# Kernel optimization log

Measured on AMD Instinct MI355X. Metric: run time of the kernel, lower is better.

The kernel has to match this reference:

```python
import jax, jax.numpy as jnp
import numpy as np

NEG_SLOPE = 0.2  # PyG GATConv default negative_slope


def gat_conv(x, src, dst, W, att_src, att_dst, bias, heads):
    """PyG-style GATConv (concat=True). src/dst already include self-loops.
    x: [N, Fin]; W: [Fin, heads*Fout]; att_*: [heads, Fout]; bias: [heads*Fout].
    """
    N = x.shape[0]
    Fout = att_src.shape[-1]
    h = (x @ W).reshape(N, heads, Fout)              # [N, H, C]
    a_s = jnp.einsum('nhc,hc->nh', h, att_src)        # [N, H]
    a_d = jnp.einsum('nhc,hc->nh', h, att_dst)        # [N, H]
    e = jax.nn.leaky_relu(a_s[src] + a_d[dst], NEG_SLOPE)   # [E, H]
    # segment softmax over destination nodes
    m = jax.lax.stop_gradient(jax.ops.segment_max(e, dst, num_segments=N))  # [N, H]
    ex = jnp.exp(e - m[dst])
    denom = jax.ops.segment_sum(ex, dst, num_segments=N)     # [N, H]
    alpha = ex / (denom[dst] + 1e-16)                          # [E, H]
    msg = h[src] * alpha[:, :, None]                           # [E, H, C]
    out = jax.ops.segment_sum(msg, dst, num_segments=N)       # [N, H, C]
    return out.reshape(N, heads * Fout) + bias


def setup_inputs() -> dict:
    key = jax.random.key(0)
    ks = jax.random.split(key, 16)
    NU, NS, D, H, CTX, B, E = 100000, 100000, 64, 2, 3, 512, 1600000
    inp = {
        'user_idx': jax.random.randint(ks[0], (B,), 0, NU),
        'context_idx': jax.random.randint(ks[1], (B, CTX), 0, NS),
        'edge_index': jax.random.randint(ks[2], (2, E), 0, NS),
        'user_emb': jax.random.normal(ks[3], (NU, D), jnp.float32),
        'service_emb': jax.random.normal(ks[4], (NS, D), jnp.float32),
        'W1': jax.random.normal(ks[5], (D, H * D), jnp.float32) / np.sqrt(D),
        'att_src1': jax.random.normal(ks[6], (H, D), jnp.float32) / np.sqrt(D),
        'att_dst1': jax.random.normal(ks[7], (H, D), jnp.float32) / np.sqrt(D),
        'b1': jnp.zeros((H * D,), jnp.float32),
        'W2': jax.random.normal(ks[8], (H * D, D), jnp.float32) / np.sqrt(H * D),
        'att_src2': jax.random.normal(ks[9], (1, D), jnp.float32) / np.sqrt(D),
        'att_dst2': jax.random.normal(ks[10], (1, D), jnp.float32) / np.sqrt(D),
        'b2': jnp.zeros((D,), jnp.float32),
        'fc_w': jax.random.normal(ks[11], (D * (CTX + 1), NS), jnp.float32) / np.sqrt(D * (CTX + 1)),
        'fc_b': jnp.zeros((NS,), jnp.float32),
    }
    return inp


def reference(user_idx, context_idx, edge_index, user_emb, service_emb,
              W1, att_src1, att_dst1, b1, W2, att_src2, att_dst2, b2, fc_w, fc_b):
    N = service_emb.shape[0]
    loops = jnp.arange(N)
    src = jnp.concatenate([edge_index[0], loops])  # add self loops (PyG default)
    dst = jnp.concatenate([edge_index[1], loops])
    user_vec = user_emb[user_idx]                                  # [B, D]
    g = gat_conv(service_emb, src, dst, W1, att_src1, att_dst1, b1, heads=2)
    g = jax.nn.elu(g)
    g = gat_conv(g, src, dst, W2, att_src2, att_dst2, b2, heads=1)  # [N, D]
    ctx = g[context_idx]                                            # [B, CTX, D]
    ctx = ctx.reshape(ctx.shape[0], -1)
    x = jnp.concatenate([user_vec, ctx], axis=1)                    # [B, D*(CTX+1)]
    return x @ fc_w + fc_b                                           # [B, num_services]
```

## Files before the change

kernel.cpp:

```cpp
#include <hip/hip_runtime.h>
#include <hip/hip_bf16.h>
#include <math.h>

#define NEG_SLOPE 0.2f

#define NPB 512
#define NPB_SH 9
#define SRC_BITS 18
#define LCAP 16384
#define BCAP 16384

typedef __attribute__((ext_vector_type(8))) short short8;
typedef __attribute__((ext_vector_type(4))) float f32x4;

__device__ __forceinline__ float leaky(float x) { return x > 0.f ? x : NEG_SLOPE * x; }

__device__ __forceinline__ unsigned short f2bf(float f) {
  unsigned u = __float_as_uint(f);
  unsigned r = (u + 0x7FFFu + ((u >> 16) & 1u)) >> 16;
  return (unsigned short)r;
}

__global__ void k_h1(const float* __restrict__ x, const float* __restrict__ W1,
                     const float* __restrict__ att_src, const float* __restrict__ att_dst,
                     unsigned short* __restrict__ h1, float* __restrict__ a_s,
                     float* __restrict__ a_d, int N) {
  __shared__ __align__(16) float W1s[64 * 128];
  __shared__ __align__(16) float xs[2][64];
  for (int i = threadIdx.x; i < 64 * 128; i += 256) W1s[i] = W1[i];
  const int ln  = threadIdx.x >> 7;
  const int col = threadIdx.x & 127;
  const int head = col >> 6;
  const int c = col & 63;
  const float as_w = att_src[head * 64 + c];
  const float ad_w = att_dst[head * 64 + c];
  __syncthreads();
  float wreg[64];
#pragma unroll
  for (int cc = 0; cc < 64; ++cc) wreg[cc] = W1s[cc * 128 + col];

  const int node0 = blockIdx.x * 32;
  for (int it = 0; it < 16; ++it) {
    const int nbase = node0 + it * 2;
    __syncthreads();
    if (threadIdx.x < 128) {
      const int nn = nbase + (threadIdx.x >> 6);
      if (nn < N) xs[threadIdx.x >> 6][threadIdx.x & 63] = x[(size_t)nn * 64 + (threadIdx.x & 63)];
    }
    __syncthreads();
    const int n = nbase + ln;
    if (n >= N) continue;
    float acc = 0.f;
#pragma unroll
    for (int q = 0; q < 16; ++q) {
      const float4 xv = *(const float4*)&xs[ln][q * 4];
      acc = fmaf(xv.x, wreg[q * 4 + 0], acc);
      acc = fmaf(xv.y, wreg[q * 4 + 1], acc);
      acc = fmaf(xv.z, wreg[q * 4 + 2], acc);
      acc = fmaf(xv.w, wreg[q * 4 + 3], acc);
    }
    h1[(size_t)n * 128 + col] = f2bf(acc);
    float vs = acc * as_w;
    float vd = acc * ad_w;
#pragma unroll
    for (int off = 32; off > 0; off >>= 1) {
      vs += __shfl_down(vs, off, 64);
      vd += __shfl_down(vd, off, 64);
    }
    if (c == 0) { a_s[n * 2 + head] = vs; a_d[n * 2 + head] = vd; }
  }
}

__global__ void k_binit(int* __restrict__ cursor, int NB) {
  const int i = blockIdx.x * 256 + threadIdx.x;
  if (i < NB) cursor[i] = i * BCAP;
}

__global__ __launch_bounds__(1024) void k_bscatter(const int* __restrict__ src,
                                                   const int* __restrict__ dst, int E, int Etot,
                                                   int epb, int* __restrict__ cursor,
                                                   unsigned* __restrict__ rec, int NB) {
  __shared__ int hist[256];
  __shared__ int cur[256];
  const int tid = threadIdx.x;
  if (tid < 256) hist[tid] = 0;
  __syncthreads();
  const int e0 = blockIdx.x * epb;
  const int e1 = min(e0 + epb, Etot);
  for (int e = e0 + tid; e < e1; e += 1024) {
    const int d = (e < E) ? dst[e] : (e - E);
    atomicAdd(&hist[d >> NPB_SH], 1);
  }
  __syncthreads();
  if (tid < NB) {
    const int c = hist[tid];
    cur[tid] = c ? atomicAdd(&cursor[tid], c) : 0;
  }
  __syncthreads();
  for (int e = e0 + tid; e < e1; e += 1024) {
    int sv, d;
    if (e < E) { sv = src[e]; d = dst[e]; } else { sv = d = e - E; }
    const int b = d >> NPB_SH;
    const int p = atomicAdd(&cur[b], 1);
    rec[p] = (unsigned)sv | ((unsigned)(d & (NPB - 1)) << SRC_BITS);
  }
}

__global__ void k_bscan2(const int* __restrict__ cursor, int* __restrict__ bucketBase,
                         int NB, int Etot, int* __restrict__ rowptr, int N) {
  __shared__ int s[256];
  const int tid = threadIdx.x;
  const int v = (tid < NB) ? (cursor[tid] - tid * BCAP) : 0;
  s[tid] = v;
  __syncthreads();
  for (int off = 1; off < 256; off <<= 1) {
    const int t = (tid >= off) ? s[tid - off] : 0;
    __syncthreads();
    s[tid] += t;
    __syncthreads();
  }
  if (tid < NB) bucketBase[tid] = s[tid] - v;
  if (tid == 0) { bucketBase[NB] = Etot; rowptr[N] = Etot; }
}

__global__ __launch_bounds__(1024) void k_bcsr(const unsigned* __restrict__ rec,
                                               const int* __restrict__ bucketBase,
                                               int* __restrict__ rowptr, int* __restrict__ adj,
                                               int N, int NB) {
  __shared__ int ldeg[NPB];
  __shared__ int s[NPB];
  __shared__ int ladj[LCAP];
  const int b = blockIdx.x;
  const int tid = threadIdx.x;
  const int o0 = bucketBase[b];
  const int cnt = bucketBase[b + 1] - o0;
  const int r0 = b * BCAP;
  if (tid < NPB) ldeg[tid] = 0;
  __syncthreads();
  for (int i = tid; i < cnt; i += 1024)
    atomicAdd(&ldeg[rec[r0 + i] >> SRC_BITS], 1);
  __syncthreads();
  int v = 0;
  if (tid < NPB) { v = ldeg[tid]; s[tid] = v; }
  __syncthreads();
  for (int off = 1; off < NPB; off <<= 1) {
    int t = 0;
    if (tid < NPB && tid >= off) t = s[tid - off];
    __syncthreads();
    if (tid < NPB) s[tid] += t;
    __syncthreads();
  }
  if (tid < NPB) {
    const int excl = s[tid] - v;
    const int node = b * NPB + tid;
    if (node < N) rowptr[node] = o0 + excl;
    ldeg[tid] = excl;
  }
  __syncthreads();
  if (cnt <= LCAP) {
    for (int i = tid; i < cnt; i += 1024) {
      const unsigned r = rec[r0 + i];
      const int p = atomicAdd(&ldeg[r >> SRC_BITS], 1);
      ladj[p] = (int)(r & ((1u << SRC_BITS) - 1));
    }
    __syncthreads();
    for (int i = tid; i < cnt; i += 1024) adj[o0 + i] = ladj[i];
  } else {
    for (int i = tid; i < cnt; i += 1024) {
      const unsigned r = rec[r0 + i];
      const int p = atomicAdd(&ldeg[r >> SRC_BITS], 1);
      adj[o0 + p] = (int)(r & ((1u << SRC_BITS) - 1));
    }
  }
}

__global__ void k_zeroflags(int* __restrict__ flagC, int* __restrict__ flag1,
                            int* __restrict__ cnt, int N) {
  const int i = blockIdx.x * 256 + threadIdx.x;
  if (i < N) { flagC[i] = 0; flag1[i] = 0; }
  if (i < 2) cnt[i] = 0;
}

__global__ void k_markC(const int* __restrict__ ctx, int nctx, int* __restrict__ flagC,
                        int* __restrict__ flag1, int* __restrict__ listC,
                        int* __restrict__ list1, int* __restrict__ cnt) {
  const int i = blockIdx.x * 256 + threadIdx.x;
  if (i >= nctx) return;
  const int n = ctx[i];
  if (atomicExch(&flagC[n], 1) == 0) {
    listC[atomicAdd(&cnt[0], 1)] = n;
    if (atomicExch(&flag1[n], 1) == 0)
      list1[atomicAdd(&cnt[1], 1)] = n;
  }
}

__global__ void k_markS1(const int* __restrict__ listC, const int* __restrict__ rowptr,
                         const int* __restrict__ adj, int* __restrict__ flag1,
                         int* __restrict__ list1, int* __restrict__ cnt) {
  const int i = blockIdx.x * 256 + threadIdx.x;
  if (i >= cnt[0]) return;
  const int n = listC[i];
  const int kb = rowptr[n], ke = rowptr[n + 1];
  for (int k = kb; k < ke; ++k) {
    const int s = adj[k];
    if (atomicExch(&flag1[s], 1) == 0)
      list1[atomicAdd(&cnt[1], 1)] = s;
  }
}

__global__ void k_gat1(const unsigned short* __restrict__ h1, const float* __restrict__ as1,
                       const float* __restrict__ ad1, const int* __restrict__ rowptr,
                       const int* __restrict__ adj, const float* __restrict__ b1,
                       float* __restrict__ g, const int* __restrict__ list1,
                       const int* __restrict__ cnt) {
  const int w = threadIdx.x >> 6;
  const int l = threadIdx.x & 63;
  const int idx = blockIdx.x * 4 + w;
  if (idx >= cnt[1]) return;
  const int n = list1[idx];
  const int half = l >> 5;
  const int q = l & 31;
  const int head = q >> 4;
  const float adh = ad1[n * 2 + head];
  float a0 = 0.f, a1 = 0.f, a2 = 0.f, a3 = 0.f, dsum = 0.f;
  const int kb = rowptr[n], ke = rowptr[n + 1];
  const int kend = ke - 1;
  for (int k = kb + half; k < ke; k += 8) {
    const int e1 = k + 2, e2 = k + 4, e3 = k + 6;
    const int s0 = adj[k];
    const int s1 = adj[min(e1, kend)];
    const int s2 = adj[min(e2, kend)];
    const int s3 = adj[min(e3, kend)];
    const float x0 = as1[s0 * 2 + head] + adh;
    const float x1 = as1[s1 * 2 + head] + adh;
    const float x2 = as1[s2 * 2 + head] + adh;
    const float x3 = as1[s3 * 2 + head] + adh;
    const uint2 u0 = *(const uint2*)(h1 + (size_t)s0 * 128 + 4 * q);
    const uint2 u1 = *(const uint2*)(h1 + (size_t)s1 * 128 + 4 * q);
    const uint2 u2 = *(const uint2*)(h1 + (size_t)s2 * 128 + 4 * q);
    const uint2 u3 = *(const uint2*)(h1 + (size_t)s3 * 128 + 4 * q);
    const float w0 = __expf(leaky(x0));
    const float w1 = (e1 < ke) ? __expf(leaky(x1)) : 0.f;
    const float w2 = (e2 < ke) ? __expf(leaky(x2)) : 0.f;
    const float w3 = (e3 < ke) ? __expf(leaky(x3)) : 0.f;
    dsum += (w0 + w1) + (w2 + w3);
    a0 = fmaf(w0, __uint_as_float(u0.x << 16), a0);
    a1 = fmaf(w0, __uint_as_float(u0.x & 0xFFFF0000u), a1);
    a2 = fmaf(w0, __uint_as_float(u0.y << 16), a2);
    a3 = fmaf(w0, __uint_as_float(u0.y & 0xFFFF0000u), a3);
    a0 = fmaf(w1, __uint_as_float(u1.x << 16), a0);
    a1 = fmaf(w1, __uint_as_float(u1.x & 0xFFFF0000u), a1);
    a2 = fmaf(w1, __uint_as_float(u1.y << 16), a2);
    a3 = fmaf(w1, __uint_as_float(u1.y & 0xFFFF0000u), a3);
    a0 = fmaf(w2, __uint_as_float(u2.x << 16), a0);
    a1 = fmaf(w2, __uint_as_float(u2.x & 0xFFFF0000u), a1);
    a2 = fmaf(w2, __uint_as_float(u2.y << 16), a2);
    a3 = fmaf(w2, __uint_as_float(u2.y & 0xFFFF0000u), a3);
    a0 = fmaf(w3, __uint_as_float(u3.x << 16), a0);
    a1 = fmaf(w3, __uint_as_float(u3.x & 0xFFFF0000u), a1);
    a2 = fmaf(w3, __uint_as_float(u3.y << 16), a2);
    a3 = fmaf(w3, __uint_as_float(u3.y & 0xFFFF0000u), a3);
  }
  a0 += __shfl_xor(a0, 32, 64);
  a1 += __shfl_xor(a1, 32, 64);
  a2 += __shfl_xor(a2, 32, 64);
  a3 += __shfl_xor(a3, 32, 64);
  dsum += __shfl_xor(dsum, 32, 64);
  if (half == 0) {
    const float inv = 1.f / (dsum + 1e-16f);
    const float4 bv = *(const float4*)(b1 + 4 * q);
    float g0 = fmaf(a0, inv, bv.x);
    float g1 = fmaf(a1, inv, bv.y);
    float g2v = fmaf(a2, inv, bv.z);
    float g3 = fmaf(a3, inv, bv.w);
    g0 = g0 > 0.f ? g0 : expm1f(g0);
    g1 = g1 > 0.f ? g1 : expm1f(g1);
    g2v = g2v > 0.f ? g2v : expm1f(g2v);
    g3 = g3 > 0.f ? g3 : expm1f(g3);
    *(float4*)(g + (size_t)n * 128 + 4 * q) = make_float4(g0, g1, g2v, g3);
  }
}

__global__ void k_h2(const float* __restrict__ g, const float* __restrict__ W2,
                     const float* __restrict__ att_s, const float* __restrict__ att_d,
                     unsigned short* __restrict__ h2, float* __restrict__ a_s,
                     float* __restrict__ a_d, const int* __restrict__ list1,
                     const int* __restrict__ cnt) {
  const int cnt1 = cnt[1];
  const int base0 = blockIdx.x * 32;
  if (base0 >= cnt1) return;
  __shared__ __align__(16) float W2s[128 * 64];
  __shared__ __align__(16) float gs[2][128];
  __shared__ float part[2][64];
  for (int i = threadIdx.x; i < 128 * 64; i += 256) W2s[i] = W2[i];
  const int col = threadIdx.x & 63;
  const int kh  = (threadIdx.x >> 6) & 1;
  const int ln  = threadIdx.x >> 7;
  const float as_w = att_s[col], ad_w = att_d[col];
  __syncthreads();
  float wreg[64];
#pragma unroll
  for (int cc = 0; cc < 64; ++cc) wreg[cc] = W2s[(kh * 64 + cc) * 64 + col];

  for (int it = 0; it < 16; ++it) {
    const int sbase = base0 + it * 2;
    __syncthreads();
    {
      const int slot = sbase + (threadIdx.x >> 7);
      if (slot < cnt1) {
        const int nn = list1[slot];
        gs[threadIdx.x >> 7][threadIdx.x & 127] = g[(size_t)nn * 128 + (threadIdx.x & 127)];
      }
    }
    __syncthreads();
    const int slot = sbase + ln;
    const int n = (slot < cnt1) ? list1[slot] : -1;
    float acc = 0.f;
    if (n >= 0) {
#pragma unroll
      for (int q = 0; q < 16; ++q) {
        const float4 gv = *(const float4*)&gs[ln][kh * 64 + q * 4];
        acc = fmaf(gv.x, wreg[q * 4 + 0], acc);
        acc = fmaf(gv.y, wreg[q * 4 + 1], acc);
        acc = fmaf(gv.z, wreg[q * 4 + 2], acc);
        acc = fmaf(gv.w, wreg[q * 4 + 3], acc);
      }
    }
    if (kh == 1) part[ln][col] = acc;
    __syncthreads();
    if (kh == 0 && n >= 0) {
      acc += part[ln][col];
      h2[(size_t)n * 64 + col] = f2bf(acc);
      float vs = acc * as_w, vd = acc * ad_w;
#pragma unroll
      for (int off = 32; off > 0; off >>= 1) {
        vs += __shfl_down(vs, off, 64);
        vd += __shfl_down(vd, off, 64);
      }
      if (col == 0) { a_s[n] = vs; a_d[n] = vd; }
    }
  }
}

__global__ void k_gat2(const unsigned short* __restrict__ h2, const float* __restrict__ as2,
                       const float* __restrict__ ad2, const int* __restrict__ rowptr,
                       const int* __restrict__ adj, const float* __restrict__ b2,
                       float* __restrict__ g2, const int* __restrict__ listC,
                       const int* __restrict__ cnt) {
  const int w = threadIdx.x >> 6;
  const int l = threadIdx.x & 63;
  const int idx = blockIdx.x * 4 + w;
  if (idx >= cnt[0]) return;
  const int n = listC[idx];
  const int half = l >> 5;
  const int q = l & 31;
  const float adh = ad2[n];
  float a0 = 0.f, a1 = 0.f, dsum = 0.f;
  const int kb = rowptr[n], ke = rowptr[n + 1];
  const int kend = ke - 1;
  for (int k = kb + half; k < ke; k += 8) {
    const int e1 = k + 2, e2 = k + 4, e3 = k + 6;
    const int s0 = adj[k];
    const int s1 = adj[min(e1, kend)];
    const int s2 = adj[min(e2, kend)];
    const int s3 = adj[min(e3, kend)];
    const float x0 = as2[s0] + adh;
    const float x1 = as2[s1] + adh;
    const float x2 = as2[s2] + adh;
    const float x3 = as2[s3] + adh;
    const unsigned u0 = *(const unsigned*)(h2 + (size_t)s0 * 64 + 2 * q);
    const unsigned u1 = *(const unsigned*)(h2 + (size_t)s1 * 64 + 2 * q);
    const unsigned u2 = *(const unsigned*)(h2 + (size_t)s2 * 64 + 2 * q);
    const unsigned u3 = *(const unsigned*)(h2 + (size_t)s3 * 64 + 2 * q);
    const float w0 = __expf(leaky(x0));
    const float w1 = (e1 < ke) ? __expf(leaky(x1)) : 0.f;
    const float w2 = (e2 < ke) ? __expf(leaky(x2)) : 0.f;
    const float w3 = (e3 < ke) ? __expf(leaky(x3)) : 0.f;
    dsum += (w0 + w1) + (w2 + w3);
    a0 = fmaf(w0, __uint_as_float(u0 << 16), a0);
    a1 = fmaf(w0, __uint_as_float(u0 & 0xFFFF0000u), a1);
    a0 = fmaf(w1, __uint_as_float(u1 << 16), a0);
    a1 = fmaf(w1, __uint_as_float(u1 & 0xFFFF0000u), a1);
    a0 = fmaf(w2, __uint_as_float(u2 << 16), a0);
    a1 = fmaf(w2, __uint_as_float(u2 & 0xFFFF0000u), a1);
    a0 = fmaf(w3, __uint_as_float(u3 << 16), a0);
    a1 = fmaf(w3, __uint_as_float(u3 & 0xFFFF0000u), a1);
  }
  a0 += __shfl_xor(a0, 32, 64);
  a1 += __shfl_xor(a1, 32, 64);
  dsum += __shfl_xor(dsum, 32, 64);
  if (half == 0) {
    const float inv = 1.f / (dsum + 1e-16f);
    const float2 bv = *(const float2*)(b2 + 2 * q);
    ((float2*)g2)[(size_t)n * 32 + q] =
        make_float2(fmaf(a0, inv, bv.x), fmaf(a1, inv, bv.y));
  }
}

__global__ void k_xmat(const int* __restrict__ user_idx, const int* __restrict__ ctx_idx,
                       const float* __restrict__ user_emb, const float* __restrict__ g2,
                       unsigned short* __restrict__ xb) {
  const int b = blockIdx.x;
  const int k = threadIdx.x;
  float v;
  if (k < 64) {
    v = user_emb[(size_t)user_idx[b] * 64 + k];
  } else {
    const int c = (k - 64) >> 6;
    v = g2[(size_t)ctx_idx[b * 3 + c] * 64 + (k & 63)];
  }
  xb[(size_t)(k >> 5) * (512 * 32) + b * 32 + (k & 31)] = f2bf(v);
}

__global__ __launch_bounds__(512) void k_fc(const unsigned short* __restrict__ xb,
                                            const float* __restrict__ fc_w,
                                            const float* __restrict__ fc_b,
                                            float* __restrict__ out, int NSRV,
                                            int ntiles, int gstride) {
  __shared__ __align__(16) unsigned short Blds[2][32 * 264];

  const int tid = threadIdx.x;
  const int w = tid >> 6;
  const int lane = tid & 63;
  const int l15 = lane & 15;
  const int kg = lane >> 4;

  if (blockIdx.x >= (unsigned)ntiles) return;

  short8 afr[4][8];
#pragma unroll
  for (int mf = 0; mf < 4; ++mf) {
    const int row = w * 64 + mf * 16 + l15;
#pragma unroll
    for (int ks = 0; ks < 8; ++ks) {
      afr[mf][ks] = *(const short8*)(xb + (size_t)ks * 16384 + row * 32 + kg * 8);
    }
  }

  const int sc = tid & 31;
  const int sk = tid >> 5;

  float v[16];
  auto loadv = [&](int t) {
    const int cg = t * 32 + sc;
    const bool okc = cg < NSRV;
#pragma unroll
    for (int i = 0; i < 16; ++i)
      v[i] = okc ? fc_w[(size_t)(sk + i * 16) * NSRV + cg] : 0.f;
  };
  auto writev = [&](int buf) {
#pragma unroll
    for (int i = 0; i < 16; ++i)
      Blds[buf][sc * 264 + sk + i * 16] = f2bf(v[i]);
  };

  loadv(blockIdx.x);
  writev(0);
  if (blockIdx.x + gstride < ntiles) loadv(blockIdx.x + gstride);
  __syncthreads();

  int cur = 0;
  for (int t = blockIdx.x; t < ntiles; t += gstride) {
    if (t + gstride < ntiles) writev(cur ^ 1);
    if (t + 2 * gstride < ntiles) loadv(t + 2 * gstride);
    const int j0 = t * 32;
#pragma unroll
    for (int nf = 0; nf < 2; ++nf) {
      short8 bfr[8];
#pragma unroll
      for (int ks = 0; ks < 8; ++ks)
        bfr[ks] = *(const short8*)&Blds[cur][(nf * 16 + l15) * 264 + ks * 32 + kg * 8];
      f32x4 acc[4];
#pragma unroll
      for (int mf = 0; mf < 4; ++mf) acc[mf] = (f32x4){0.f, 0.f, 0.f, 0.f};
#pragma unroll
      for (int ks = 0; ks < 8; ++ks)
#pragma unroll
        for (int mf = 0; mf < 4; ++mf)
          acc[mf] = __builtin_amdgcn_mfma_f32_16x16x32_bf16(bfr[ks], afr[mf][ks], acc[mf], 0, 0, 0);
      const int jc = j0 + nf * 16 + kg * 4;
      if (j0 + 32 <= NSRV) {
        const float4 bias = *(const float4*)(fc_b + jc);
#pragma unroll
        for (int mf = 0; mf < 4; ++mf) {
          const int row = w * 64 + mf * 16 + l15;
          float4 o;
          o.x = acc[mf][0] + bias.x;
          o.y = acc[mf][1] + bias.y;
          o.z = acc[mf][2] + bias.z;
          o.w = acc[mf][3] + bias.w;
          *(float4*)(out + (size_t)row * NSRV + jc) = o;
        }
      } else {
#pragma unroll
        for (int mf = 0; mf < 4; ++mf) {
          const int row = w * 64 + mf * 16 + l15;
#pragma unroll
          for (int r = 0; r < 4; ++r) {
            const int j = jc + r;
            if (j < NSRV) out[(size_t)row * NSRV + j] = acc[mf][r] + fc_b[j];
          }
        }
      }
    }
    __syncthreads();
    cur ^= 1;
  }
}

extern "C" void kernel_launch(void* const* d_in, const int* in_sizes, int n_in,
                              void* d_out, int out_size, void* d_ws, size_t ws_size,
                              hipStream_t stream) {
  const int* user_idx    = (const int*)d_in[0];
  const int* context_idx = (const int*)d_in[1];
  const int* edge_index  = (const int*)d_in[2];
  const float* user_emb  = (const float*)d_in[3];
  const float* service_emb = (const float*)d_in[4];
  const float* W1        = (const float*)d_in[5];
  const float* att_src1  = (const float*)d_in[6];
  const float* att_dst1  = (const float*)d_in[7];
  const float* b1        = (const float*)d_in[8];
  const float* W2        = (const float*)d_in[9];
  const float* att_src2  = (const float*)d_in[10];
  const float* att_dst2  = (const float*)d_in[11];
  const float* b2        = (const float*)d_in[12];
  const float* fc_w      = (const float*)d_in[13];
  const float* fc_b      = (const float*)d_in[14];
  float* out = (float*)d_out;

  const int B    = in_sizes[0];
  const int E    = in_sizes[2] / 2;
  const int N    = in_sizes[4] / 64;
  const int NSRV = in_sizes[14];
  const int Etot = E + N;
  const int NCTX = in_sizes[1];

  const int* edge_src = edge_index;
  const int* edge_dst = edge_index + E;

  char* ws = (char*)d_ws;
  size_t off = 0;
  auto alloc = [&](size_t bytes) {
    void* p = ws + off;
    off = (off + bytes + 255) & ~(size_t)255;
    return p;
  };
  const int NB = (N + NPB - 1) >> NPB_SH;
  unsigned short* h1 = (unsigned short*)alloc((size_t)N * 128 * 2);
  float* g      = (float*)alloc((size_t)N * 128 * 4);
  float* as1    = (float*)alloc((size_t)N * 2 * 4);
  float* ad1    = (float*)alloc((size_t)N * 2 * 4);
  float* as2    = (float*)alloc((size_t)N * 4);
  float* ad2    = (float*)alloc((size_t)N * 4);
  int*   rowptr = (int*)alloc((size_t)(N + 1) * 4);
  int*   adj    = (int*)alloc((size_t)Etot * 4);
  unsigned* rec = (unsigned*)alloc((size_t)NB * BCAP * 4);
  int* bucketBase   = (int*)alloc(257 * 4);
  int* bucketCursor = (int*)alloc(256 * 4);
  int* flagC  = (int*)alloc((size_t)N * 4);
  int* flag1  = (int*)alloc((size_t)N * 4);
  int* listC  = (int*)alloc((size_t)NCTX * 4);
  int* list1  = (int*)alloc((size_t)N * 4);
  int* cnt    = (int*)alloc(2 * 4);
  unsigned short* xb = (unsigned short*)alloc((size_t)512 * 256 * 2);
  unsigned short* h2 = h1;
  float* g2 = g;
  (void)ws_size;

  const int NBLK2 = 256;
  const int epb = (Etot + NBLK2 - 1) / NBLK2;
  const int nblk_N = (N + 255) / 256;

  k_h1<<<(N + 31) / 32, 256, 0, stream>>>(service_emb, W1, att_src1, att_dst1, h1, as1, ad1, N);

  k_binit<<<1, 256, 0, stream>>>(bucketCursor, NB);
  k_bscatter<<<NBLK2, 1024, 0, stream>>>(edge_src, edge_dst, E, Etot, epb, bucketCursor, rec, NB);
  k_bscan2<<<1, 256, 0, stream>>>(bucketCursor, bucketBase, NB, Etot, rowptr, N);
  k_bcsr<<<NB, 1024, 0, stream>>>(rec, bucketBase, rowptr, adj, N, NB);

  k_zeroflags<<<nblk_N, 256, 0, stream>>>(flagC, flag1, cnt, N);
  k_markC<<<(NCTX + 255) / 256, 256, 0, stream>>>(context_idx, NCTX, flagC, flag1, listC, list1, cnt);
  k_markS1<<<(NCTX + 255) / 256, 256, 0, stream>>>(listC, rowptr, adj, flag1, list1, cnt);

  k_gat1<<<(N + 3) / 4, 256, 0, stream>>>(h1, as1, ad1, rowptr, adj, b1, g, list1, cnt);

  k_h2<<<(N + 31) / 32, 256, 0, stream>>>(g, W2, att_src2, att_dst2, h2, as2, ad2, list1, cnt);

  k_gat2<<<(NCTX + 3) / 4, 256, 0, stream>>>(h2, as2, ad2, rowptr, adj, b2, g2, listC, cnt);

  k_xmat<<<512, 256, 0, stream>>>(user_idx, context_idx, user_emb, g2, xb);

  const int nfct = (NSRV + 31) / 32;
  const int grid = 512;
  k_fc<<<grid, 512, 0, stream>>>(xb, fc_w, fc_b, out, NSRV, nfct, grid);
}
```

Before: 307.2 us.

## Preload node tile in k_h1, merge init kernels, use nontemporal fc loads/stores

k_h1 now loads all 32 nodes' input rows into shared memory once with float4 loads, which removes the two block barriers per iteration. The bucket-cursor init and flag zeroing kernels are merged into a single launch to cut launch overhead. The final FC kernel reads fc_w and writes the output with nontemporal loads and stores, so this streaming traffic does not pollute the cache. The changes are small and independent, and the shared-memory footprint of k_h1 grows.

Measured after the change: 295.5 us. 1.04x faster.

```diff
diff --git a/kernel.cpp b/kernel.cpp
--- a/kernel.cpp
+++ b/kernel.cpp
@@ -26,10 +26,16 @@
                      unsigned short* __restrict__ h1, float* __restrict__ a_s,
                      float* __restrict__ a_d, int N) {
   __shared__ __align__(16) float W1s[64 * 128];
-  __shared__ __align__(16) float xs[2][64];
-  for (int i = threadIdx.x; i < 64 * 128; i += 256) W1s[i] = W1[i];
-  const int ln  = threadIdx.x >> 7;
-  const int col = threadIdx.x & 127;
+  __shared__ __align__(16) float xs[32][64];
+  const int tid = threadIdx.x;
+  for (int i = tid; i < 64 * 128; i += 256) W1s[i] = W1[i];
+  const int node0 = blockIdx.x * 32;
+  for (int i = tid; i < 512; i += 256) {
+    const int nn = node0 + (i >> 4);
+    if (nn < N) ((float4*)xs)[i] = *(const float4*)(x + (size_t)nn * 64 + (i & 15) * 4);
+  }
+  const int ln  = tid >> 7;
+  const int col = tid & 127;
   const int head = col >> 6;
   const int c = col & 63;
   const float as_w = att_src[head * 64 + c];
@@ -39,21 +45,14 @@
 #pragma unroll
   for (int cc = 0; cc < 64; ++cc) wreg[cc] = W1s[cc * 128 + col];
 
-  const int node0 = blockIdx.x * 32;
   for (int it = 0; it < 16; ++it) {
-    const int nbase = node0 + it * 2;
-    __syncthreads();
-    if (threadIdx.x < 128) {
-      const int nn = nbase + (threadIdx.x >> 6);
-      if (nn < N) xs[threadIdx.x >> 6][threadIdx.x & 63] = x[(size_t)nn * 64 + (threadIdx.x & 63)];
-    }
-    __syncthreads();
-    const int n = nbase + ln;
+    const int slot = it * 2 + ln;
+    const int n = node0 + slot;
     if (n >= N) continue;
     float acc = 0.f;
 #pragma unroll
     for (int q = 0; q < 16; ++q) {
-      const float4 xv = *(const float4*)&xs[ln][q * 4];
+      const float4 xv = *(const float4*)&xs[slot][q * 4];
       acc = fmaf(xv.x, wreg[q * 4 + 0], acc);
       acc = fmaf(xv.y, wreg[q * 4 + 1], acc);
       acc = fmaf(xv.z, wreg[q * 4 + 2], acc);
@@ -71,9 +70,12 @@
   }
 }
 
-__global__ void k_binit(int* __restrict__ cursor, int NB) {
+__global__ void k_init(int* __restrict__ cursor, int NB, int* __restrict__ flagC,
+                       int* __restrict__ flag1, int* __restrict__ cnt, int N) {
   const int i = blockIdx.x * 256 + threadIdx.x;
   if (i < NB) cursor[i] = i * BCAP;
+  if (i < N) { flagC[i] = 0; flag1[i] = 0; }
+  if (i < 2) cnt[i] = 0;
 }
 
 __global__ __launch_bounds__(1024) void k_bscatter(const int* __restrict__ src,
@@ -172,13 +174,6 @@
       adj[o0 + p] = (int)(r & ((1u << SRC_BITS) - 1));
     }
   }
-}
-
-__global__ void k_zeroflags(int* __restrict__ flagC, int* __restrict__ flag1,
-                            int* __restrict__ cnt, int N) {
-  const int i = blockIdx.x * 256 + threadIdx.x;
-  if (i < N) { flagC[i] = 0; flag1[i] = 0; }
-  if (i < 2) cnt[i] = 0;
 }
 
 __global__ void k_markC(const int* __restrict__ ctx, int nctx, int* __restrict__ flagC,
@@ -446,7 +441,7 @@
     const bool okc = cg < NSRV;
 #pragma unroll
     for (int i = 0; i < 16; ++i)
-      v[i] = okc ? fc_w[(size_t)(sk + i * 16) * NSRV + cg] : 0.f;
+      v[i] = okc ? __builtin_nontemporal_load(fc_w + (size_t)(sk + i * 16) * NSRV + cg) : 0.f;
   };
   auto writev = [&](int buf) {
 #pragma unroll
@@ -484,12 +479,12 @@
 #pragma unroll
         for (int mf = 0; mf < 4; ++mf) {
           const int row = w * 64 + mf * 16 + l15;
-          float4 o;
-          o.x = acc[mf][0] + bias.x;
-          o.y = acc[mf][1] + bias.y;
-          o.z = acc[mf][2] + bias.z;
-          o.w = acc[mf][3] + bias.w;
-          *(float4*)(out + (size_t)row * NSRV + jc) = o;
+          f32x4 o;
+          o[0] = acc[mf][0] + bias.x;
+          o[1] = acc[mf][1] + bias.y;
+          o[2] = acc[mf][2] + bias.z;
+          o[3] = acc[mf][3] + bias.w;
+          __builtin_nontemporal_store(o, (f32x4*)(out + (size_t)row * NSRV + jc));
         }
       } else {
 #pragma unroll
@@ -534,6 +529,7 @@
   const int NSRV = in_sizes[14];
   const int Etot = E + N;
   const int NCTX = in_sizes[1];
+  (void)B;
 
   const int* edge_src = edge_index;
   const int* edge_dst = edge_index + E;
@@ -571,14 +567,14 @@
   const int epb = (Etot + NBLK2 - 1) / NBLK2;
   const int nblk_N = (N + 255) / 256;
 
+  k_init<<<nblk_N, 256, 0, stream>>>(bucketCursor, NB, flagC, flag1, cnt, N);
+
   k_h1<<<(N + 31) / 32, 256, 0, stream>>>(service_emb, W1, att_src1, att_dst1, h1, as1, ad1, N);
 
-  k_binit<<<1, 256, 0, stream>>>(bucketCursor, NB);
   k_bscatter<<<NBLK2, 1024, 0, stream>>>(edge_src, edge_dst, E, Etot, epb, bucketCursor, rec, NB);
   k_bscan2<<<1, 256, 0, stream>>>(bucketCursor, bucketBase, NB, Etot, rowptr, N);
   k_bcsr<<<NB, 1024, 0, stream>>>(rec, bucketBase, rowptr, adj, N, NB);
 
-  k_zeroflags<<<nblk_N, 256, 0, stream>>>(flagC, flag1, cnt, N);
   k_markC<<<(NCTX + 255) / 256, 256, 0, stream>>>(context_idx, NCTX, flagC, flag1, listC, list1, cnt);
   k_markS1<<<(NCTX + 255) / 256, 256, 0, stream>>>(listC, rowptr, adj, flag1, list1, cnt);
 
```
